# Kernel optimization log

Hardware: AMD Instinct MI355X
Metric: run time of the kernel (lower is better)

## Reference

```python
import jax, jax.numpy as jnp
import numpy as np

B, N, C, H = 4, 1024, 1024, 16
HD = C // H
SCALE = HD ** -0.5


def _init_linear(key, out_dim, in_dim):
    # torch nn.Linear default init: U(-1/sqrt(in), 1/sqrt(in)) for weight and bias
    kw, kb = jax.random.split(key)
    bound = 1.0 / np.sqrt(in_dim)
    W = jax.random.uniform(kw, (out_dim, in_dim), jnp.float32, -bound, bound)
    b = jax.random.uniform(kb, (out_dim,), jnp.float32, -bound, bound)
    return W, b


def setup_inputs() -> dict:
    key = jax.random.key(0)
    ks = jax.random.split(key, 5)
    x = jax.random.normal(ks[0], (B, N, C), jnp.float32)
    # NdLinear qkv: Linear(N->N) along seq axis, then Linear(C->3C) along channel axis
    Wq0, bq0 = _init_linear(ks[1], N, N)
    Wq1, bq1 = _init_linear(ks[2], 3 * C, C)
    # NdLinear proj: Linear(N->N) along seq axis, then Linear(C->C) along channel axis
    Wp0, bp0 = _init_linear(ks[3], N, N)
    Wp1, bp1 = _init_linear(ks[4], C, C)
    return {"x": x, "Wq0": Wq0, "bq0": bq0, "Wq1": Wq1, "bq1": bq1,
            "Wp0": Wp0, "bp0": bp0, "Wp1": Wp1, "bp1": bp1}


def _ndlinear(x, W0, b0, W1, b1):
    # NdLinear over (seq, channel): apply Linear along axis 1, then axis 2.
    # torch Linear: y = x @ W.T + b
    x = jnp.einsum('bnc,mn->bmc', x, W0) + b0[None, :, None]   # seq axis
    x = jnp.einsum('bnc,dc->bnd', x, W1) + b1                  # channel axis
    return x


def reference(x, Wq0, bq0, Wq1, bq1, Wp0, bp0, Wp1, bp1):
    qkv = _ndlinear(x, Wq0, bq0, Wq1, bq1)                     # (B, N, 3C)
    qkv = qkv.reshape(B, N, 3, H, HD).transpose(2, 0, 3, 1, 4) # (3, B, H, N, HD)
    q, k, v = qkv[0], qkv[1], qkv[2]
    attn = jnp.einsum('bhnd,bhmd->bhnm', q, k) * SCALE         # (B, H, N, N)
    attn = jax.nn.softmax(attn, axis=-1)
    out = jnp.einsum('bhnm,bhmd->bhnd', attn, v)               # (B, H, N, HD)
    out = out.transpose(0, 2, 1, 3).reshape(B, N, C)
    out = _ndlinear(out, Wp0, bp0, Wp1, bp1)
    return out
```

## Files before the change

### kernel.cpp

```cpp
#include <hip/hip_runtime.h>
#include <hip/hip_bf16.h>
#include <stdint.h>

typedef __bf16 bf16;
typedef __bf16 bf16x4 __attribute__((ext_vector_type(4)));
typedef __bf16 bf16x8 __attribute__((ext_vector_type(8)));
typedef float f32x4 __attribute__((ext_vector_type(4)));

#define B_ 4
#define N_ 1024
#define C_ 1024
#define H_ 16
#define MEG (1u << 20)

__device__ __forceinline__ uint32_t lds_off(const void* p) {
    return (uint32_t)(uintptr_t)p;
}
__device__ __forceinline__ void g2l16(const void* g, uint32_t lds_byte) {
    __builtin_amdgcn_global_load_lds(
        (const __attribute__((address_space(1))) unsigned int*)(uintptr_t)g,
        (__attribute__((address_space(3))) unsigned int*)(uintptr_t)lds_byte,
        16, 0, 0);
}

__global__ __launch_bounds__(256) void prep_k(
    const float* __restrict__ x, bf16* __restrict__ xT,
    const float* __restrict__ s0, bf16* __restrict__ d0,
    const float* __restrict__ s1, bf16* __restrict__ d1,
    const float* __restrict__ s2, bf16* __restrict__ d2,
    const float* __restrict__ s3, bf16* __restrict__ d3)
{
    __shared__ bf16 t[64][66];
    const int bid = blockIdx.x;
    const int tid = threadIdx.x;
    if (bid < 3072) {
        const float* s; bf16* d; int base;
        if (bid < 512)       { s = s0; d = d0; base = 0; }
        else if (bid < 2048) { s = s1; d = d1; base = 512; }
        else if (bid < 2560) { s = s2; d = d2; base = 2048; }
        else                 { s = s3; d = d3; base = 2560; }
        int i = ((bid - base) * 256 + tid) * 8;
        float4 a = *(const float4*)(s + i);
        float4 b = *(const float4*)(s + i + 4);
        bf16x8 r;
        r[0] = (bf16)a.x; r[1] = (bf16)a.y; r[2] = (bf16)a.z; r[3] = (bf16)a.w;
        r[4] = (bf16)b.x; r[5] = (bf16)b.y; r[6] = (bf16)b.z; r[7] = (bf16)b.w;
        *(bf16x8*)(d + i) = r;
        return;
    }
    const int idx = bid - 3072;
    const int c0 = (idx & 15) * 64, n0 = ((idx >> 4) & 15) * 64, b = idx >> 8;
    {
        int nl = tid >> 2, seg = tid & 3;
        const float* src = x + ((size_t)b * N_ + n0 + nl) * C_ + c0 + seg * 16;
#pragma unroll
        for (int i = 0; i < 4; ++i) {
            float4 v = *(const float4*)(src + i * 4);
            t[nl][seg * 16 + i * 4 + 0] = (bf16)v.x;
            t[nl][seg * 16 + i * 4 + 1] = (bf16)v.y;
            t[nl][seg * 16 + i * 4 + 2] = (bf16)v.z;
            t[nl][seg * 16 + i * 4 + 3] = (bf16)v.w;
        }
    }
    __syncthreads();
    {
        int cl = tid >> 2, seg = tid & 3;
        bf16* dst = xT + ((size_t)b * C_ + c0 + cl) * N_ + n0 + seg * 16;
        bf16x8 o0, o1;
#pragma unroll
        for (int j = 0; j < 8; ++j) o0[j] = t[seg * 16 + j][cl];
#pragma unroll
        for (int j = 0; j < 8; ++j) o1[j] = t[seg * 16 + 8 + j][cl];
        *(bf16x8*)dst = o0;
        *(bf16x8*)(dst + 8) = o1;
    }
}

template <int BIAS, bool OF32, bool VSPLIT>
__global__ __launch_bounds__(512) void gemm_k(
    const bf16* __restrict__ A, const bf16* __restrict__ Bm,
    const float* __restrict__ bias, void* __restrict__ Cv,
    bf16* __restrict__ vT,
    int M, int Nn, int K, long long sA, long long sB, long long sC)
{
    __shared__ bf16 smem[2][2][128 * 64];

    const int tid = threadIdx.x;
    const int lane = tid & 63, wid = tid >> 6;
    const int lr = lane & 15, lg = lane >> 4;
    const int wr = wid >> 2, wc = wid & 3;
    const int m0 = blockIdx.y * 128, n0 = blockIdx.x * 128;

    const bf16* Ab = A + (size_t)blockIdx.z * sA;
    const bf16* Bb = Bm + (size_t)blockIdx.z * sB;

    const uint32_t a_lds0 = lds_off(&smem[0][0][0]);
    const uint32_t b_lds0 = lds_off(&smem[0][1][0]);
    const uint32_t bufstride = 2 * 128 * 64 * 2;

    auto stage = [&](int kt, int buf) {
#pragma unroll
        for (int half = 0; half < 2; ++half) {
            int it = tid + half * 512;
            int r = it >> 3, ch = it & 7;
            int sch = ch ^ (r & 7);
            g2l16(Ab + (size_t)(m0 + r) * K + kt * 64 + sch * 8,
                  a_lds0 + buf * bufstride + it * 16);
            g2l16(Bb + (size_t)(n0 + r) * K + kt * 64 + sch * 8,
                  b_lds0 + buf * bufstride + it * 16);
        }
    };

    f32x4 acc[4][2];
#pragma unroll
    for (int i = 0; i < 4; ++i)
#pragma unroll
        for (int j = 0; j < 2; ++j) { f32x4 z = {0.f,0.f,0.f,0.f}; acc[i][j] = z; }

    stage(0, 0);
    __syncthreads();

    const int nt = K >> 6;
    for (int t = 0; t < nt; ++t) {
        int buf = t & 1;
        if (t + 1 < nt) stage(t + 1, buf ^ 1);
        const bf16* As = &smem[buf][0][0];
        const bf16* Bs = &smem[buf][1][0];
#pragma unroll
        for (int s = 0; s < 2; ++s) {
            bf16x8 af[4], bfr[2];
#pragma unroll
            for (int mi = 0; mi < 4; ++mi) {
                int row = wr * 64 + mi * 16 + lr;
                int slot = (s * 4 + lg) ^ (row & 7);
                af[mi] = *(const bf16x8*)(As + row * 64 + slot * 8);
            }
#pragma unroll
            for (int ni = 0; ni < 2; ++ni) {
                int row = wc * 32 + ni * 16 + lr;
                int slot = (s * 4 + lg) ^ (row & 7);
                bfr[ni] = *(const bf16x8*)(Bs + row * 64 + slot * 8);
            }
#pragma unroll
            for (int mi = 0; mi < 4; ++mi)
#pragma unroll
                for (int ni = 0; ni < 2; ++ni)
                    acc[mi][ni] = __builtin_amdgcn_mfma_f32_16x16x32_bf16(
                        af[mi], bfr[ni], acc[mi][ni], 0, 0, 0);
        }
        __syncthreads();
    }

#pragma unroll
    for (int mi = 0; mi < 4; ++mi)
#pragma unroll
        for (int ni = 0; ni < 2; ++ni) {
            int col = n0 + wc * 32 + ni * 16 + lr;
            if constexpr (VSPLIT) {
                if (col >= 2048) {
                    float bv = bias[col];
                    bf16x4 w;
#pragma unroll
                    for (int r = 0; r < 4; ++r) w[r] = (bf16)(acc[mi][ni][r] + bv);
                    int row0 = m0 + wr * 64 + mi * 16 + lg * 4;
                    int bb = row0 >> 10, n = row0 & 1023;
                    *(bf16x4*)(vT + (size_t)bb * MEG +
                               (size_t)(col - 2048) * 1024 + n) = w;
                    continue;
                }
            }
#pragma unroll
            for (int r = 0; r < 4; ++r) {
                int row = m0 + wr * 64 + mi * 16 + lg * 4 + r;
                float bv = (BIAS == 0) ? bias[row] : bias[col];
                float v = acc[mi][ni][r] + bv;
                if constexpr (OF32)
                    ((float*)Cv + (size_t)blockIdx.z * sC)[(size_t)row * Nn + col] = v;
                else
                    ((bf16*)Cv + (size_t)blockIdx.z * sC)[(size_t)row * Nn + col] = (bf16)v;
            }
        }
}

__global__ __launch_bounds__(256) void attn_k(
    const bf16* __restrict__ qkv, const bf16* __restrict__ vT,
    bf16* __restrict__ aoT)
{
    __shared__ bf16 Ks[2][4096];
    __shared__ bf16 Vs[2][4096];
    __shared__ bf16 pbuf[4][2048];

    const int tid = threadIdx.x;
    const int lane = tid & 63, wid = tid >> 6;
    const int lr = lane & 15, lg = lane >> 4;
    const int bid = blockIdx.x;
    const int qt = bid >> 6, hb = bid & 63;
    const int b = hb >> 4, h = hb & 15;
    const int qrow0 = qt * 128 + wid * 32;
    const int hoff = h * 64;
    const bf16* qkvb = qkv + (size_t)b * (N_ * 3 * C_);
    const bf16* vTb  = vT + (size_t)b * MEG;

    bf16x8 qfA[2], qfB[2];
#pragma unroll
    for (int kk = 0; kk < 2; ++kk) {
        qfA[kk] = *(const bf16x8*)(qkvb + (size_t)(qrow0 + lr) * 3072 +
                                   hoff + kk * 32 + lg * 8);
        qfB[kk] = *(const bf16x8*)(qkvb + (size_t)(qrow0 + 16 + lr) * 3072 +
                                   hoff + kk * 32 + lg * 8);
#pragma unroll
        for (int j = 0; j < 8; ++j) {
            qfA[kk][j] = (bf16)((float)qfA[kk][j] * 0.18033688f);
            qfB[kk][j] = (bf16)((float)qfB[kk][j] * 0.18033688f);
        }
    }

    const uint32_t ks0 = lds_off(&Ks[0][0]);
    const uint32_t vs0 = lds_off(&Vs[0][0]);

    auto stageK = [&](int kt, int buf) {
#pragma unroll
        for (int hh = 0; hh < 2; ++hh) {
            int it = tid + hh * 256;
            int key = it >> 3, ch = it & 7;
            int sch = ch ^ (key & 7);
            g2l16(qkvb + (size_t)(kt * 64 + key) * 3072 + C_ + hoff + sch * 8,
                  ks0 + buf * 8192 + it * 16);
        }
    };
    auto stageV = [&](int kt, int buf) {
#pragma unroll
        for (int hh = 0; hh < 2; ++hh) {
            int it = tid + hh * 256;
            int d = it >> 3, ch = it & 7;
            int sch = ch ^ (d & 7);
            g2l16(vTb + (size_t)(hoff + d) * 1024 + kt * 64 + sch * 8,
                  vs0 + buf * 8192 + it * 16);
        }
    };

    float lsumA = 0.f, lsumB = 0.f;
    f32x4 oA[4], oB[4];
#pragma unroll
    for (int i = 0; i < 4; ++i) {
        f32x4 z = {0.f,0.f,0.f,0.f};
        oA[i] = z; oB[i] = z;
    }

    char* prowA = (char*)&pbuf[wid][0] + lr * 128;
    char* prowB = (char*)&pbuf[wid][0] + (16 + lr) * 128;
    const int swz = (lr & 7) << 4;

    stageK(0, 0);
    stageV(0, 0);
    __syncthreads();

    for (int kt = 0; kt < 16; ++kt) {
        int buf = kt & 1;
        if (kt + 1 < 16) {
            stageK(kt + 1, buf ^ 1);
            stageV(kt + 1, buf ^ 1);
        }

        f32x4 sA[4], sB[4];
        __builtin_amdgcn_s_setprio(1);
#pragma unroll
        for (int st = 0; st < 4; ++st) {
            f32x4 zA = {0.f, 0.f, 0.f, 0.f};
            f32x4 zB = {0.f, 0.f, 0.f, 0.f};
#pragma unroll
            for (int kk = 0; kk < 2; ++kk) {
                int row = st * 16 + lr;
                int slot = (kk * 4 + lg) ^ (row & 7);
                bf16x8 kf = *(const bf16x8*)(&Ks[buf][row * 64 + slot * 8]);
                zA = __builtin_amdgcn_mfma_f32_16x16x32_bf16(kf, qfA[kk], zA, 0, 0, 0);
                zB = __builtin_amdgcn_mfma_f32_16x16x32_bf16(kf, qfB[kk], zB, 0, 0, 0);
            }
            sA[st] = zA; sB[st] = zB;
        }
        __builtin_amdgcn_s_setprio(0);

#pragma unroll
        for (int st = 0; st < 4; ++st) {
            bf16x4 wA, wB;
#pragma unroll
            for (int r = 0; r < 4; ++r) {
                float eA = __builtin_amdgcn_exp2f(sA[st][r]);
                float eB = __builtin_amdgcn_exp2f(sB[st][r]);
                wA[r] = (bf16)eA; lsumA += eA;
                wB[r] = (bf16)eB; lsumB += eB;
            }
            *(bf16x4*)(prowA + ((st * 32 + lg * 8) ^ swz)) = wA;
            *(bf16x4*)(prowB + ((st * 32 + lg * 8) ^ swz)) = wB;
        }

        bf16x8 pfA[2], pfB[2];
        pfA[0] = *(const bf16x8*)(prowA + ((lg * 16) ^ swz));
        pfA[1] = *(const bf16x8*)(prowA + ((64 + lg * 16) ^ swz));
        pfB[0] = *(const bf16x8*)(prowB + ((lg * 16) ^ swz));
        pfB[1] = *(const bf16x8*)(prowB + ((64 + lg * 16) ^ swz));

        __builtin_amdgcn_s_setprio(1);
#pragma unroll
        for (int dt = 0; dt < 4; ++dt) {
            int row = dt * 16 + lr;
            bf16x8 v0 = *(const bf16x8*)(&Vs[buf][row * 64 + ((lg ^ (lr & 7)) * 8)]);
            bf16x8 v1 = *(const bf16x8*)(&Vs[buf][row * 64 + (((4 + lg) ^ (lr & 7)) * 8)]);
            oA[dt] = __builtin_amdgcn_mfma_f32_16x16x32_bf16(pfA[0], v0, oA[dt], 0, 0, 0);
            oA[dt] = __builtin_amdgcn_mfma_f32_16x16x32_bf16(pfA[1], v1, oA[dt], 0, 0, 0);
            oB[dt] = __builtin_amdgcn_mfma_f32_16x16x32_bf16(pfB[0], v0, oB[dt], 0, 0, 0);
            oB[dt] = __builtin_amdgcn_mfma_f32_16x16x32_bf16(pfB[1], v1, oB[dt], 0, 0, 0);
        }
        __builtin_amdgcn_s_setprio(0);

        __syncthreads();
    }

    lsumA += __shfl_xor(lsumA, 16, 64);
    lsumA += __shfl_xor(lsumA, 32, 64);
    lsumB += __shfl_xor(lsumB, 16, 64);
    lsumB += __shfl_xor(lsumB, 32, 64);
    float rtotA = 1.0f / lsumA, rtotB = 1.0f / lsumB;
    float rcpoA[4], rcpoB[4];
#pragma unroll
    for (int r = 0; r < 4; ++r) {
        rcpoA[r] = __shfl(rtotA, lg * 4 + r, 64);
        rcpoB[r] = __shfl(rtotB, lg * 4 + r, 64);
    }

#pragma unroll
    for (int dt = 0; dt < 4; ++dt) {
        bf16x4 ovA, ovB;
#pragma unroll
        for (int r = 0; r < 4; ++r) {
            ovA[r] = (bf16)(oA[dt][r] * rcpoA[r]);
            ovB[r] = (bf16)(oB[dt][r] * rcpoB[r]);
        }
        size_t c = (size_t)b * C_ + hoff + dt * 16 + lr;
        *(bf16x4*)(aoT + c * N_ + qrow0 + lg * 4) = ovA;
        *(bf16x4*)(aoT + c * N_ + qrow0 + 16 + lg * 4) = ovB;
    }
}

extern "C" void kernel_launch(void* const* d_in, const int* in_sizes, int n_in,
                              void* d_out, int out_size, void* d_ws, size_t ws_size,
                              hipStream_t stream) {
    (void)in_sizes; (void)n_in; (void)out_size; (void)ws_size;
    const float* x   = (const float*)d_in[0];
    const float* Wq0 = (const float*)d_in[1];
    const float* bq0 = (const float*)d_in[2];
    const float* Wq1 = (const float*)d_in[3];
    const float* bq1 = (const float*)d_in[4];
    const float* Wp0 = (const float*)d_in[5];
    const float* bp0 = (const float*)d_in[6];
    const float* Wp1 = (const float*)d_in[7];
    const float* bp1 = (const float*)d_in[8];

    bf16* ws   = (bf16*)d_ws;
    bf16* xT   = ws;
    bf16* Wq0b = ws + 4 * MEG;
    bf16* Wq1b = ws + 5 * MEG;
    bf16* Wp0b = ws + 8 * MEG;
    bf16* Wp1b = ws + 9 * MEG;
    bf16* y1   = ws + 10 * MEG;
    bf16* y2   = ws + 14 * MEG;
    bf16* vT   = xT;
    bf16* aoT  = y1;
    bf16* z1   = y2;
    float* outp = (float*)d_out;

    const long long s1M = (long long)N_ * C_;

    prep_k<<<dim3(4096), 256, 0, stream>>>(x, xT, Wq0, Wq0b, Wq1, Wq1b,
                                           Wp0, Wp0b, Wp1, Wp1b);

    gemm_k<0, false, false><<<dim3(8, 8, 4), 512, 0, stream>>>(
        Wq0b, xT, bq0, y1, nullptr, 1024, 1024, 1024, 0LL, s1M, s1M);
    gemm_k<1, false, true><<<dim3(24, 32, 1), 512, 0, stream>>>(
        y1, Wq1b, bq1, y2, vT, 4096, 3072, 1024, 0LL, 0LL, 0LL);
    attn_k<<<dim3(512), 256, 0, stream>>>(y2, vT, aoT);
    gemm_k<0, false, false><<<dim3(8, 8, 4), 512, 0, stream>>>(
        Wp0b, aoT, bp0, z1, nullptr, 1024, 1024, 1024, 0LL, s1M, s1M);
    gemm_k<1, true, false><<<dim3(8, 32, 1), 512, 0, stream>>>(
        z1, Wp1b, bp1, outp, nullptr, 4096, 1024, 1024, 0LL, 0LL, 0LL);
}
```

Before: 118.6 us.

## Halve GEMM tile width and software-pipeline attention QK^T with a deeper V ring

Result: no change. 118.1 us (-0.4%).

```diff
diff --git a/kernel.cpp b/kernel.cpp
--- a/kernel.cpp
+++ b/kernel.cpp
@@ -77,35 +77,41 @@
 }
 
 template <int BIAS, bool OF32, bool VSPLIT>
-__global__ __launch_bounds__(512) void gemm_k(
+__global__ __launch_bounds__(256) void gemm64_k(
     const bf16* __restrict__ A, const bf16* __restrict__ Bm,
     const float* __restrict__ bias, void* __restrict__ Cv,
     bf16* __restrict__ vT,
     int M, int Nn, int K, long long sA, long long sB, long long sC)
 {
-    __shared__ bf16 smem[2][2][128 * 64];
+    __shared__ bf16 smem[2][192 * 64];
 
     const int tid = threadIdx.x;
     const int lane = tid & 63, wid = tid >> 6;
     const int lr = lane & 15, lg = lane >> 4;
-    const int wr = wid >> 2, wc = wid & 3;
-    const int m0 = blockIdx.y * 128, n0 = blockIdx.x * 128;
+    const int wr = wid >> 1, wc = wid & 1;
+    const int m0 = blockIdx.y * 128, n0 = blockIdx.x * 64;
 
     const bf16* Ab = A + (size_t)blockIdx.z * sA;
     const bf16* Bb = Bm + (size_t)blockIdx.z * sB;
 
-    const uint32_t a_lds0 = lds_off(&smem[0][0][0]);
-    const uint32_t b_lds0 = lds_off(&smem[0][1][0]);
-    const uint32_t bufstride = 2 * 128 * 64 * 2;
+    const uint32_t a_lds0 = lds_off(&smem[0][0]);
+    const uint32_t b_lds0 = a_lds0 + 128 * 64 * 2;
+    const uint32_t bufstride = 192 * 64 * 2;
 
     auto stage = [&](int kt, int buf) {
 #pragma unroll
-        for (int half = 0; half < 2; ++half) {
-            int it = tid + half * 512;
+        for (int h = 0; h < 4; ++h) {
+            int it = tid + h * 256;
             int r = it >> 3, ch = it & 7;
             int sch = ch ^ (r & 7);
             g2l16(Ab + (size_t)(m0 + r) * K + kt * 64 + sch * 8,
                   a_lds0 + buf * bufstride + it * 16);
+        }
+#pragma unroll
+        for (int h = 0; h < 2; ++h) {
+            int it = tid + h * 256;
+            int r = it >> 3, ch = it & 7;
+            int sch = ch ^ (r & 7);
             g2l16(Bb + (size_t)(n0 + r) * K + kt * 64 + sch * 8,
                   b_lds0 + buf * bufstride + it * 16);
         }
@@ -124,8 +130,8 @@
     for (int t = 0; t < nt; ++t) {
         int buf = t & 1;
         if (t + 1 < nt) stage(t + 1, buf ^ 1);
-        const bf16* As = &smem[buf][0][0];
-        const bf16* Bs = &smem[buf][1][0];
+        const bf16* As = &smem[buf][0];
+        const bf16* Bs = &smem[buf][128 * 64];
 #pragma unroll
         for (int s = 0; s < 2; ++s) {
             bf16x8 af[4], bfr[2];
@@ -187,7 +193,7 @@
     bf16* __restrict__ aoT)
 {
     __shared__ bf16 Ks[2][4096];
-    __shared__ bf16 Vs[2][4096];
+    __shared__ bf16 Vs[3][4096];
     __shared__ bf16 pbuf[4][2048];
 
     const int tid = threadIdx.x;
@@ -239,6 +245,26 @@
         }
     };
 
+    auto qkt = [&](int kt, f32x4* SA, f32x4* SB) {
+        const bf16* Kbase = &Ks[kt & 1][0];
+        __builtin_amdgcn_s_setprio(1);
+#pragma unroll
+        for (int st = 0; st < 4; ++st) {
+            f32x4 zA = {0.f, 0.f, 0.f, 0.f};
+            f32x4 zB = {0.f, 0.f, 0.f, 0.f};
+#pragma unroll
+            for (int kk = 0; kk < 2; ++kk) {
+                int row = st * 16 + lr;
+                int slot = (kk * 4 + lg) ^ (row & 7);
+                bf16x8 kf = *(const bf16x8*)(Kbase + row * 64 + slot * 8);
+                zA = __builtin_amdgcn_mfma_f32_16x16x32_bf16(kf, qfA[kk], zA, 0, 0, 0);
+                zB = __builtin_amdgcn_mfma_f32_16x16x32_bf16(kf, qfB[kk], zB, 0, 0, 0);
+            }
+            SA[st] = zA; SB[st] = zB;
+        }
+        __builtin_amdgcn_s_setprio(0);
+    };
+
     float lsumA = 0.f, lsumB = 0.f;
     f32x4 oA[4], oB[4];
 #pragma unroll
@@ -251,34 +277,20 @@
     char* prowB = (char*)&pbuf[wid][0] + (16 + lr) * 128;
     const int swz = (lr & 7) << 4;
 
-    stageK(0, 0);
-    stageV(0, 0);
-    __syncthreads();
+    stageK(0, 0); stageV(0, 0);
+    stageK(1, 1); stageV(1, 1);
+    asm volatile("s_waitcnt vmcnt(4)" ::: "memory");
+    __builtin_amdgcn_s_barrier();
+
+    f32x4 sA[4], sB[4];
+    qkt(0, sA, sB);
+    __builtin_amdgcn_s_barrier();
 
     for (int kt = 0; kt < 16; ++kt) {
-        int buf = kt & 1;
-        if (kt + 1 < 16) {
-            stageK(kt + 1, buf ^ 1);
-            stageV(kt + 1, buf ^ 1);
-        }
-
-        f32x4 sA[4], sB[4];
-        __builtin_amdgcn_s_setprio(1);
-#pragma unroll
-        for (int st = 0; st < 4; ++st) {
-            f32x4 zA = {0.f, 0.f, 0.f, 0.f};
-            f32x4 zB = {0.f, 0.f, 0.f, 0.f};
-#pragma unroll
-            for (int kk = 0; kk < 2; ++kk) {
-                int row = st * 16 + lr;
-                int slot = (kk * 4 + lg) ^ (row & 7);
-                bf16x8 kf = *(const bf16x8*)(&Ks[buf][row * 64 + slot * 8]);
-                zA = __builtin_amdgcn_mfma_f32_16x16x32_bf16(kf, qfA[kk], zA, 0, 0, 0);
-                zB = __builtin_amdgcn_mfma_f32_16x16x32_bf16(kf, qfB[kk], zB, 0, 0, 0);
-            }
-            sA[st] = zA; sB[st] = zB;
-        }
-        __builtin_amdgcn_s_setprio(0);
+        if (kt + 2 < 16) {
+            stageK(kt + 2, kt & 1);
+            stageV(kt + 2, (kt + 2) % 3);
+        }
 
 #pragma unroll
         for (int st = 0; st < 4; ++st) {
@@ -294,18 +306,29 @@
             *(bf16x4*)(prowB + ((st * 32 + lg * 8) ^ swz)) = wB;
         }
 
+        f32x4 nA[4], nB[4];
+        if (kt + 1 < 16) {
+            if (kt + 2 < 16)
+                asm volatile("s_waitcnt vmcnt(4)" ::: "memory");
+            else
+                asm volatile("s_waitcnt vmcnt(0)" ::: "memory");
+            __builtin_amdgcn_s_barrier();
+            qkt(kt + 1, nA, nB);
+        }
+
         bf16x8 pfA[2], pfB[2];
         pfA[0] = *(const bf16x8*)(prowA + ((lg * 16) ^ swz));
         pfA[1] = *(const bf16x8*)(prowA + ((64 + lg * 16) ^ swz));
         pfB[0] = *(const bf16x8*)(prowB + ((lg * 16) ^ swz));
         pfB[1] = *(const bf16x8*)(prowB + ((64 + lg * 16) ^ swz));
 
+        const bf16* Vbase = &Vs[kt % 3][0];
         __builtin_amdgcn_s_setprio(1);
 #pragma unroll
         for (int dt = 0; dt < 4; ++dt) {
             int row = dt * 16 + lr;
-            bf16x8 v0 = *(const bf16x8*)(&Vs[buf][row * 64 + ((lg ^ (lr & 7)) * 8)]);
-            bf16x8 v1 = *(const bf16x8*)(&Vs[buf][row * 64 + (((4 + lg) ^ (lr & 7)) * 8)]);
+            bf16x8 v0 = *(const bf16x8*)(Vbase + row * 64 + ((lg ^ (lr & 7)) * 8));
+            bf16x8 v1 = *(const bf16x8*)(Vbase + row * 64 + (((4 + lg) ^ (lr & 7)) * 8));
             oA[dt] = __builtin_amdgcn_mfma_f32_16x16x32_bf16(pfA[0], v0, oA[dt], 0, 0, 0);
             oA[dt] = __builtin_amdgcn_mfma_f32_16x16x32_bf16(pfA[1], v1, oA[dt], 0, 0, 0);
             oB[dt] = __builtin_amdgcn_mfma_f32_16x16x32_bf16(pfB[0], v0, oB[dt], 0, 0, 0);
@@ -313,7 +336,10 @@
         }
         __builtin_amdgcn_s_setprio(0);
 
-        __syncthreads();
+        __builtin_amdgcn_s_barrier();
+
+#pragma unroll
+        for (int i = 0; i < 4; ++i) { sA[i] = nA[i]; sB[i] = nB[i]; }
     }
 
     lsumA += __shfl_xor(lsumA, 16, 64);
@@ -374,13 +400,13 @@
     prep_k<<<dim3(4096), 256, 0, stream>>>(x, xT, Wq0, Wq0b, Wq1, Wq1b,
                                            Wp0, Wp0b, Wp1, Wp1b);
 
-    gemm_k<0, false, false><<<dim3(8, 8, 4), 512, 0, stream>>>(
+    gemm64_k<0, false, false><<<dim3(16, 8, 4), 256, 0, stream>>>(
         Wq0b, xT, bq0, y1, nullptr, 1024, 1024, 1024, 0LL, s1M, s1M);
-    gemm_k<1, false, true><<<dim3(24, 32, 1), 512, 0, stream>>>(
+    gemm64_k<1, false, true><<<dim3(48, 32, 1), 256, 0, stream>>>(
         y1, Wq1b, bq1, y2, vT, 4096, 3072, 1024, 0LL, 0LL, 0LL);
     attn_k<<<dim3(512), 256, 0, stream>>>(y2, vT, aoT);
-    gemm_k<0, false, false><<<dim3(8, 8, 4), 512, 0, stream>>>(
+    gemm64_k<0, false, false><<<dim3(16, 8, 4), 256, 0, stream>>>(
         Wp0b, aoT, bp0, z1, nullptr, 1024, 1024, 1024, 0LL, s1M, s1M);
-    gemm_k<1, true, false><<<dim3(8, 32, 1), 512, 0, stream>>>(
+    gemm64_k<1, true, false><<<dim3(16, 32, 1), 256, 0, stream>>>(
         z1, Wp1b, bp1, outp, nullptr, 4096, 1024, 1024, 0LL, 0LL, 0LL);
 }
```
